# Kernel optimization log

Hardware: AMD Instinct MI355X
Metric: run time of the kernel (lower is better)

The kernel has to match this reference:

```python
import jax, jax.numpy as jnp
import numpy as np

N, C, IMG, HEADS = 512, 3, 32, 4
F = C * IMG * IMG          # 3072 node feature dim
E = 4096                   # edges without self loops
EPS = 1e-5                 # BatchNorm eps
SLOPE = 0.2                # GATv2 LeakyReLU negative slope


def bn(x, g, b, m, v):
    # eval-mode BatchNorm2d over channel dim 1
    inv = g / jnp.sqrt(v + EPS)
    return x * inv[None, :, None, None] + (b - m * inv)[None, :, None, None]


def conv1x1(x, W, b):
    # W: [out_c, in_c]
    return jnp.einsum('bchw,oc->bohw', x, W) + b[None, :, None, None]


def setup_inputs():
    key = jax.random.key(0)
    ks = jax.random.split(key, 32)
    inp = {}
    inp['x'] = jax.random.normal(ks[0], (N, C, IMG, IMG), jnp.float32)
    src = jax.random.randint(ks[1], (E,), 0, N)
    off = jax.random.randint(ks[2], (E,), 1, N)
    inp['edge_index'] = jnp.stack([src, (src + off) % N]).astype(jnp.int32)  # no self loops

    def w(k, shape, fan_in):
        return jax.random.normal(k, shape, jnp.float32) / np.sqrt(fan_in)

    i = 3
    def nk():
        nonlocal i; i += 1; return ks[i - 1]
    # grapher fc1: Conv2d(C,C,1)+BN
    inp['fc1_W'] = w(nk(), (C, C), C); inp['fc1_b'] = jnp.zeros((C,), jnp.float32)
    inp['bn1_g'] = jnp.ones((C,), jnp.float32); inp['bn1_b'] = jnp.zeros((C,), jnp.float32)
    inp['bn1_m'] = 0.1 * jax.random.normal(nk(), (C,), jnp.float32)
    inp['bn1_v'] = jax.random.uniform(nk(), (C,), jnp.float32, 0.5, 1.5)
    # GATv2Conv(F, F, heads=HEADS): lin_l, lin_r [F, HEADS*F] with bias, att [HEADS, F], out bias
    inp['Wl'] = w(nk(), (F, HEADS * F), F); inp['bl'] = jnp.zeros((HEADS * F,), jnp.float32)
    inp['Wr'] = w(nk(), (F, HEADS * F), F); inp['br'] = jnp.zeros((HEADS * F,), jnp.float32)
    inp['att'] = w(nk(), (HEADS, F), F)
    inp['gat_b'] = jnp.zeros((HEADS * F,), jnp.float32)
    # grapher fc2: Conv2d(C*HEADS, C, 1)+BN
    inp['fc2_W'] = w(nk(), (C, C * HEADS), C * HEADS); inp['fc2_b'] = jnp.zeros((C,), jnp.float32)
    inp['bn2_g'] = jnp.ones((C,), jnp.float32); inp['bn2_b'] = jnp.zeros((C,), jnp.float32)
    inp['bn2_m'] = 0.1 * jax.random.normal(nk(), (C,), jnp.float32)
    inp['bn2_v'] = jax.random.uniform(nk(), (C,), jnp.float32, 0.5, 1.5)
    # FFN fc1 / fc2 (C->C 1x1 conv + BN)
    inp['ffn1_W'] = w(nk(), (C, C), C); inp['ffn1_b'] = jnp.zeros((C,), jnp.float32)
    inp['bnf1_g'] = jnp.ones((C,), jnp.float32); inp['bnf1_b'] = jnp.zeros((C,), jnp.float32)
    inp['bnf1_m'] = 0.1 * jax.random.normal(nk(), (C,), jnp.float32)
    inp['bnf1_v'] = jax.random.uniform(nk(), (C,), jnp.float32, 0.5, 1.5)
    inp['ffn2_W'] = w(nk(), (C, C), C); inp['ffn2_b'] = jnp.zeros((C,), jnp.float32)
    inp['bnf2_g'] = jnp.ones((C,), jnp.float32); inp['bnf2_b'] = jnp.zeros((C,), jnp.float32)
    inp['bnf2_m'] = 0.1 * jax.random.normal(nk(), (C,), jnp.float32)
    inp['bnf2_v'] = jax.random.uniform(nk(), (C,), jnp.float32, 0.5, 1.5)
    return inp


def reference(x, edge_index, fc1_W, fc1_b, bn1_g, bn1_b, bn1_m, bn1_v,
              Wl, bl, Wr, br, att, gat_b,
              fc2_W, fc2_b, bn2_g, bn2_b, bn2_m, bn2_v,
              ffn1_W, ffn1_b, bnf1_g, bnf1_b, bnf1_m, bnf1_v,
              ffn2_W, ffn2_b, bnf2_g, bnf2_b, bnf2_m, bnf2_v):
    shortcut = x
    h = bn(conv1x1(x, fc1_W, fc1_b), bn1_g, bn1_b, bn1_m, bn1_v)
    hf = h.reshape(N, F)
    xl = (hf @ Wl + bl).reshape(N, HEADS, F)  # source transform
    xr = (hf @ Wr + br).reshape(N, HEADS, F)  # target transform
    # add self loops (PyG GATv2Conv default)
    loops = jnp.arange(N, dtype=edge_index.dtype)
    src = jnp.concatenate([edge_index[0], loops])
    dst = jnp.concatenate([edge_index[1], loops])
    # GATv2 edge scores: a . LeakyReLU(xl_j + xr_i)
    e = jax.nn.leaky_relu(xl[src] + xr[dst], negative_slope=SLOPE)  # [E+N, HEADS, F]
    logits = jnp.einsum('ehf,hf->eh', e, att)
    mx = jax.ops.segment_max(logits, dst, num_segments=N)
    ex = jnp.exp(logits - jax.lax.stop_gradient(mx)[dst])
    denom = jax.ops.segment_sum(ex, dst, num_segments=N)
    alpha = ex / denom[dst]                                          # segment softmax over targets
    agg = jax.ops.segment_sum(xl[src] * alpha[:, :, None], dst, num_segments=N)  # [N, HEADS, F]
    g_out = (agg.reshape(N, HEADS * F) + gat_b).reshape(N, C * HEADS, IMG, IMG)
    g = bn(conv1x1(g_out, fc2_W, fc2_b), bn2_g, bn2_b, bn2_m, bn2_v) + shortcut
    # FFN with residual
    f = jax.nn.relu(bn(conv1x1(g, ffn1_W, ffn1_b), bnf1_g, bnf1_b, bnf1_m, bnf1_v))
    f = bn(conv1x1(f, ffn2_W, ffn2_b), bnf2_g, bnf2_b, bnf2_m, bnf2_v)
    return f + g
```

## Files before the change

### kernel.cpp

```cpp
#include <hip/hip_runtime.h>

#define N_NODES 512
#define FDIM    3072
#define HEADS   4
#define HFD     12288
#define E_IN    4096
#define E_TOT   4608
#define EPSV    1e-5f
#define SLOPE   0.2f

typedef unsigned short u16;
typedef unsigned int   u32;

typedef short s16x8 __attribute__((ext_vector_type(8)));
typedef float f32x4 __attribute__((ext_vector_type(4)));

__device__ __forceinline__ u16 f2bf(float f){
  u32 u = __builtin_bit_cast(u32, f);
  u = (u + 0x7fffu + ((u >> 16) & 1u)) >> 16;
  return (u16)u;
}
__device__ __forceinline__ float bf2f(u16 h){
  return __builtin_bit_cast(float, ((u32)h) << 16);
}
__device__ __forceinline__ float bflo(u32 p){
  return __builtin_bit_cast(float, p << 16);
}
__device__ __forceinline__ float bfhi(u32 p){
  return __builtin_bit_cast(float, p & 0xffff0000u);
}

__device__ __forceinline__ void gl_lds16(const u16* g, u16* l){
  __builtin_amdgcn_global_load_lds(
      (const __attribute__((address_space(1))) unsigned int*)g,
      (__attribute__((address_space(3))) unsigned int*)l, 16, 0, 0);
}

__global__ void k_fc1(const float* __restrict__ x, const float* __restrict__ W,
                      const float* __restrict__ b, const float* __restrict__ g,
                      const float* __restrict__ bb, const float* __restrict__ m,
                      const float* __restrict__ v, u16* __restrict__ hf,
                      int* __restrict__ cnt){
  int id = blockIdx.x * 256 + threadIdx.x;
  if (id < 512) cnt[id] = 0;
  int n = id >> 10, p = id & 1023;
  float x0 = x[n * FDIM + p];
  float x1 = x[n * FDIM + 1024 + p];
  float x2 = x[n * FDIM + 2048 + p];
#pragma unroll
  for (int c = 0; c < 3; ++c){
    float t = b[c] + W[c*3+0]*x0 + W[c*3+1]*x1 + W[c*3+2]*x2;
    float inv = g[c] * rsqrtf(v[c] + EPSV);
    float o = t * inv + (bb[c] - m[c] * inv);
    hf[n * FDIM + c * 1024 + p] = f2bf(o);
  }
}

__global__ __launch_bounds__(256, 2) void k_gemm(
    const u16* __restrict__ hf, const float* __restrict__ Wl,
    const float* __restrict__ bl, const float* __restrict__ Wr,
    const float* __restrict__ br, u16* __restrict__ xl, u16* __restrict__ xr){
  __shared__ u16 As[512 * 32];
  __shared__ u16 Bs[64 * 40];

  const int tid  = threadIdx.x;
  const int wave = tid >> 6, lane = tid & 63;
  const int quad = lane >> 4, l16 = lane & 15;
  const int n0 = blockIdx.x * 64;

  const float* Wg; const float* biasp; u16* outp; int cb;
  if (n0 < HFD){ Wg = Wl; biasp = bl; outp = xl; cb = n0; }
  else         { Wg = Wr; biasp = br; outp = xr; cb = n0 - HFD; }

  const u16* ga = hf + (size_t)(wave * 128 + (lane >> 2)) * FDIM
                     + (((lane & 3) ^ ((lane >> 3) & 3)) << 3);
  u16* la = As + wave * 8 * 512;

  const int bn = tid & 63, bkh = tid >> 6;
  const float* gb = Wg + (size_t)bkh * 8 * HFD + (cb + bn);
  u16* wb = Bs + bn * 40 + bkh * 8;

  const u16* raf = As + (size_t)(wave * 128 + l16) * 32 + ((quad ^ ((l16 >> 1) & 3)) << 3);
  const u16* rbf = Bs + l16 * 40 + quad * 8;

  f32x4 acc[8][4];
#pragma unroll
  for (int i = 0; i < 8; ++i)
#pragma unroll
    for (int j = 0; j < 4; ++j) acc[i][j] = (f32x4){0.f, 0.f, 0.f, 0.f};

  float bv[8];
#pragma unroll
  for (int j = 0; j < 8; ++j) bv[j] = gb[(size_t)j * HFD];

  for (int ks = 0; ks < 96; ++ks){
    __syncthreads();
#pragma unroll
    for (int i = 0; i < 8; ++i)
      gl_lds16(ga + (size_t)i * 16 * FDIM + ks * 32, la + i * 512);
    u32 pk0 = (u32)f2bf(bv[0]) | ((u32)f2bf(bv[1]) << 16);
    u32 pk1 = (u32)f2bf(bv[2]) | ((u32)f2bf(bv[3]) << 16);
    u32 pk2 = (u32)f2bf(bv[4]) | ((u32)f2bf(bv[5]) << 16);
    u32 pk3 = (u32)f2bf(bv[6]) | ((u32)f2bf(bv[7]) << 16);
    *(uint4*)wb = make_uint4(pk0, pk1, pk2, pk3);
    __syncthreads();

    s16x8 af[8], bfr[4];
#pragma unroll
    for (int i = 0; i < 8; ++i)
      af[i] = __builtin_bit_cast(s16x8, *(const uint4*)(raf + i * 512));
#pragma unroll
    for (int j = 0; j < 4; ++j)
      bfr[j] = __builtin_bit_cast(s16x8, *(const uint4*)(rbf + j * 640));

    const int kn = (ks < 95 ? ks + 1 : ks) * 32;
#pragma unroll
    for (int j = 0; j < 8; ++j) bv[j] = gb[(size_t)(kn + j) * HFD];

#pragma unroll
    for (int i = 0; i < 8; ++i)
#pragma unroll
      for (int j = 0; j < 4; ++j)
        acc[i][j] = __builtin_amdgcn_mfma_f32_16x16x32_bf16(af[i], bfr[j], acc[i][j], 0, 0, 0);
  }

  float bj[4];
#pragma unroll
  for (int j = 0; j < 4; ++j) bj[j] = biasp[cb + j * 16 + l16];
#pragma unroll
  for (int i = 0; i < 8; ++i){
    int mrow = wave * 128 + i * 16 + quad * 4;
#pragma unroll
    for (int r = 0; r < 4; ++r){
      u16* orow = outp + (size_t)(mrow + r) * HFD + cb + l16;
#pragma unroll
      for (int j = 0; j < 4; ++j)
        orow[j * 16] = f2bf(acc[i][j][r] + bj[j]);
    }
  }
}

__global__ void k_logits(const int* __restrict__ ei, const u16* __restrict__ xl,
                         const u16* __restrict__ xr, const float* __restrict__ att,
                         float* __restrict__ logits, int* __restrict__ cnt){
  int e = blockIdx.x;
  int h = threadIdx.x >> 6, lane = threadIdx.x & 63;
  int s, d;
  if (e < E_IN){ s = ei[e]; d = ei[E_IN + e]; } else { s = e - E_IN; d = s; }
  if (threadIdx.x == 0) atomicAdd(&cnt[d], 1);
  const u16* xlp = xl + (size_t)s * HFD + h * FDIM;
  const u16* xrp = xr + (size_t)d * HFD + h * FDIM;
  const float* ap = att + h * FDIM;
  float acc = 0.f;
#pragma unroll
  for (int it = 0; it < 6; ++it){
    int f = it * 512 + lane * 8;
    uint4 a = *(const uint4*)(xlp + f);
    uint4 b = *(const uint4*)(xrp + f);
    float4 w0 = *(const float4*)(ap + f);
    float4 w1 = *(const float4*)(ap + f + 4);
    float v0 = bflo(a.x) + bflo(b.x); v0 = v0 > 0.f ? v0 : SLOPE * v0;
    float v1 = bfhi(a.x) + bfhi(b.x); v1 = v1 > 0.f ? v1 : SLOPE * v1;
    float v2 = bflo(a.y) + bflo(b.y); v2 = v2 > 0.f ? v2 : SLOPE * v2;
    float v3 = bfhi(a.y) + bfhi(b.y); v3 = v3 > 0.f ? v3 : SLOPE * v3;
    float v4 = bflo(a.z) + bflo(b.z); v4 = v4 > 0.f ? v4 : SLOPE * v4;
    float v5 = bfhi(a.z) + bfhi(b.z); v5 = v5 > 0.f ? v5 : SLOPE * v5;
    float v6 = bflo(a.w) + bflo(b.w); v6 = v6 > 0.f ? v6 : SLOPE * v6;
    float v7 = bfhi(a.w) + bfhi(b.w); v7 = v7 > 0.f ? v7 : SLOPE * v7;
    acc += v0 * w0.x + v1 * w0.y + v2 * w0.z + v3 * w0.w;
    acc += v4 * w1.x + v5 * w1.y + v6 * w1.z + v7 * w1.w;
  }
#pragma unroll
  for (int o = 32; o > 0; o >>= 1) acc += __shfl_down(acc, o);
  if (lane == 0) logits[e * 4 + h] = acc;
}

__global__ void k_scan(const int* __restrict__ cnt, int* __restrict__ off,
                       int* __restrict__ cursor){
  __shared__ int s[512];
  int t = threadIdx.x;
  int v = cnt[t];
  s[t] = v;
  __syncthreads();
  for (int d = 1; d < 512; d <<= 1){
    int add = (t >= d) ? s[t - d] : 0;
    __syncthreads();
    s[t] += add;
    __syncthreads();
  }
  int exc = s[t] - v;
  off[t] = exc;
  cursor[t] = exc;
}

__global__ void k_scatter(const int* __restrict__ ei, int* __restrict__ cursor,
                          int* __restrict__ elist){
  int e = blockIdx.x * 256 + threadIdx.x;
  if (e >= E_TOT) return;
  int d = (e < E_IN) ? ei[E_IN + e] : (e - E_IN);
  int pos = atomicAdd(&cursor[d], 1);
  elist[pos] = e;
}

__global__ void k_softmax(const int* __restrict__ cnt, const int* __restrict__ off,
                          const int* __restrict__ elist, const float* __restrict__ logits,
                          float* __restrict__ alpha){
  int i = blockIdx.x;
  int lane = threadIdx.x;
  int deg = cnt[i], st = off[i];
#pragma unroll
  for (int h = 0; h < 4; ++h){
    float mx = -1e30f;
    for (int j = lane; j < deg; j += 64){
      int e = elist[st + j];
      mx = fmaxf(mx, logits[e * 4 + h]);
    }
#pragma unroll
    for (int o = 32; o > 0; o >>= 1) mx = fmaxf(mx, __shfl_down(mx, o));
    mx = __shfl(mx, 0);
    float sm = 0.f;
    for (int j = lane; j < deg; j += 64){
      int e = elist[st + j];
      sm += __expf(logits[e * 4 + h] - mx);
    }
#pragma unroll
    for (int o = 32; o > 0; o >>= 1) sm += __shfl_down(sm, o);
    sm = __shfl(sm, 0);
    float rs = 1.f / sm;
    for (int j = lane; j < deg; j += 64){
      int e = elist[st + j];
      alpha[e * 4 + h] = __expf(logits[e * 4 + h] - mx) * rs;
    }
  }
}

__global__ void k_agg(const int* __restrict__ ei, const int* __restrict__ cnt,
                      const int* __restrict__ off, const int* __restrict__ elist,
                      const float* __restrict__ alpha, const u16* __restrict__ xl,
                      float* __restrict__ agg){
  int b = blockIdx.x;
  int dst = b >> 2, h = b & 3;
  int deg = cnt[dst], st = off[dst];
  int t = threadIdx.x;
#pragma unroll
  for (int c = 0; c < 3; ++c){
    int f = c * 1024 + t * 4;
    float a0 = 0.f, a1 = 0.f, a2 = 0.f, a3 = 0.f;
    for (int j = 0; j < deg; ++j){
      int e = elist[st + j];
      int s = (e < E_IN) ? ei[e] : (e - E_IN);
      float al = alpha[e * 4 + h];
      ushort4 xv = *(const ushort4*)(xl + (size_t)s * HFD + h * FDIM + f);
      a0 += al * bf2f(xv.x);
      a1 += al * bf2f(xv.y);
      a2 += al * bf2f(xv.z);
      a3 += al * bf2f(xv.w);
    }
    float4* op = (float4*)(agg + (size_t)dst * HFD + h * FDIM + f);
    *op = make_float4(a0, a1, a2, a3);
  }
}

__global__ void k_final(const float* __restrict__ agg, const float* __restrict__ gat_b,
                        const float* __restrict__ W2, const float* __restrict__ b2,
                        const float* __restrict__ g2, const float* __restrict__ bb2,
                        const float* __restrict__ m2, const float* __restrict__ v2,
                        const float* __restrict__ W3, const float* __restrict__ b3,
                        const float* __restrict__ g3, const float* __restrict__ bb3,
                        const float* __restrict__ m3, const float* __restrict__ v3,
                        const float* __restrict__ W4, const float* __restrict__ b4,
                        const float* __restrict__ g4, const float* __restrict__ bb4,
                        const float* __restrict__ m4, const float* __restrict__ v4,
                        const float* __restrict__ x, float* __restrict__ out){
  int id = blockIdx.x * 256 + threadIdx.x;
  int n = id >> 10, p = id & 1023;
  float a[12];
#pragma unroll
  for (int o = 0; o < 12; ++o)
    a[o] = agg[(size_t)n * HFD + o * 1024 + p] + gat_b[o * 1024 + p];
  float g[3];
#pragma unroll
  for (int c = 0; c < 3; ++c){
    float t = b2[c];
#pragma unroll
    for (int o = 0; o < 12; ++o) t += W2[c * 12 + o] * a[o];
    float inv = g2[c] * rsqrtf(v2[c] + EPSV);
    g[c] = t * inv + (bb2[c] - m2[c] * inv) + x[n * FDIM + c * 1024 + p];
  }
  float f1[3];
#pragma unroll
  for (int c = 0; c < 3; ++c){
    float t = b3[c] + W3[c*3+0]*g[0] + W3[c*3+1]*g[1] + W3[c*3+2]*g[2];
    float inv = g3[c] * rsqrtf(v3[c] + EPSV);
    float vv = t * inv + (bb3[c] - m3[c] * inv);
    f1[c] = fmaxf(vv, 0.f);
  }
#pragma unroll
  for (int c = 0; c < 3; ++c){
    float t = b4[c] + W4[c*3+0]*f1[0] + W4[c*3+1]*f1[1] + W4[c*3+2]*f1[2];
    float inv = g4[c] * rsqrtf(v4[c] + EPSV);
    out[n * FDIM + c * 1024 + p] = t * inv + (bb4[c] - m4[c] * inv) + g[c];
  }
}

extern "C" void kernel_launch(void* const* d_in, const int* in_sizes, int n_in,
                              void* d_out, int out_size, void* d_ws, size_t ws_size,
                              hipStream_t stream){
  (void)in_sizes; (void)n_in; (void)out_size; (void)ws_size;
  const float* x     = (const float*)d_in[0];
  const int*   ei    = (const int*)d_in[1];
  const float* fc1_W = (const float*)d_in[2];
  const float* fc1_b = (const float*)d_in[3];
  const float* bn1_g = (const float*)d_in[4];
  const float* bn1_b = (const float*)d_in[5];
  const float* bn1_m = (const float*)d_in[6];
  const float* bn1_v = (const float*)d_in[7];
  const float* Wl    = (const float*)d_in[8];
  const float* bl    = (const float*)d_in[9];
  const float* Wr    = (const float*)d_in[10];
  const float* br    = (const float*)d_in[11];
  const float* att   = (const float*)d_in[12];
  const float* gat_b = (const float*)d_in[13];
  const float* fc2_W = (const float*)d_in[14];
  const float* fc2_b = (const float*)d_in[15];
  const float* bn2_g = (const float*)d_in[16];
  const float* bn2_b = (const float*)d_in[17];
  const float* bn2_m = (const float*)d_in[18];
  const float* bn2_v = (const float*)d_in[19];
  const float* ffn1_W= (const float*)d_in[20];
  const float* ffn1_b= (const float*)d_in[21];
  const float* bnf1_g= (const float*)d_in[22];
  const float* bnf1_b= (const float*)d_in[23];
  const float* bnf1_m= (const float*)d_in[24];
  const float* bnf1_v= (const float*)d_in[25];
  const float* ffn2_W= (const float*)d_in[26];
  const float* ffn2_b= (const float*)d_in[27];
  const float* bnf2_g= (const float*)d_in[28];
  const float* bnf2_b= (const float*)d_in[29];
  const float* bnf2_m= (const float*)d_in[30];
  const float* bnf2_v= (const float*)d_in[31];

  char* w = (char*)d_ws;
  u16*   hf     = (u16*)(w);
  u16*   xl     = (u16*)(w + 3145728);
  u16*   xr     = (u16*)(w + 15728640);
  float* logits = (float*)(w + 28311552);
  float* alpha  = (float*)(w + 28385280);
  int*   cnt    = (int*)(w + 28459008);
  int*   offp   = (int*)(w + 28461056);
  int*   cursor = (int*)(w + 28463104);
  int*   elist  = (int*)(w + 28465152);
  float* agg    = (float*)(w + 28483584);

  k_fc1<<<2048, 256, 0, stream>>>(x, fc1_W, fc1_b, bn1_g, bn1_b, bn1_m, bn1_v, hf, cnt);
  k_gemm<<<384, 256, 0, stream>>>(hf, Wl, bl, Wr, br, xl, xr);
  k_logits<<<E_TOT, 256, 0, stream>>>(ei, xl, xr, att, logits, cnt);
  k_scan<<<1, 512, 0, stream>>>(cnt, offp, cursor);
  k_scatter<<<18, 256, 0, stream>>>(ei, cursor, elist);
  k_softmax<<<512, 64, 0, stream>>>(cnt, offp, elist, logits, alpha);
  k_agg<<<2048, 256, 0, stream>>>(ei, cnt, offp, elist, alpha, xl, agg);
  k_final<<<2048, 256, 0, stream>>>(agg, gat_b, fc2_W, fc2_b, bn2_g, bn2_b, bn2_m, bn2_v,
                                    ffn1_W, ffn1_b, bnf1_g, bnf1_b, bnf1_m, bnf1_v,
                                    ffn2_W, ffn2_b, bnf2_g, bnf2_b, bnf2_m, bnf2_v,
                                    x, (float*)d_out);
}
```

Measured before the change: 553.4 us.

## Double-buffer GEMM with M-split tiles, fuse scan/scatter and agg/final kernels

The projection GEMM now splits M into two halves per block (768 blocks, smaller accumulators, launch bounds 3). It double-buffers LDS so the next k-slice loads overlap the MFMA work, and uses one barrier per step plus a grouped tile order. The scan and scatter kernels merge into one kernel that uses an LDS cursor. Aggregation and the fc2/FFN epilogue merge into a per-node kernel, which removes the float agg buffer round trip. The risks are fewer blocks and more registers in the fused aggregation (48 accumulators per thread), and serial atomics in the single-block scatter.

```diff
diff --git a/kernel.cpp b/kernel.cpp
--- a/kernel.cpp
+++ b/kernel.cpp
@@ -56,80 +56,104 @@
   }
 }
 
-__global__ __launch_bounds__(256, 2) void k_gemm(
+__global__ __launch_bounds__(256, 3) void k_gemm(
     const u16* __restrict__ hf, const float* __restrict__ Wl,
     const float* __restrict__ bl, const float* __restrict__ Wr,
     const float* __restrict__ br, u16* __restrict__ xl, u16* __restrict__ xr){
-  __shared__ u16 As[512 * 32];
-  __shared__ u16 Bs[64 * 40];
+  __shared__ u16 As[2][256 * 32];
+  __shared__ u16 Bs[2][64 * 40];
 
   const int tid  = threadIdx.x;
   const int wave = tid >> 6, lane = tid & 63;
   const int quad = lane >> 4, l16 = lane & 15;
-  const int n0 = blockIdx.x * 64;
+
+  const int g = blockIdx.x;
+  const int ntile = (g >> 4) * 8 + (g & 7);
+  const int mhalf = (g >> 3) & 1;
+  const int n0 = ntile * 64;
+  const int rbase = mhalf * 256;
 
   const float* Wg; const float* biasp; u16* outp; int cb;
   if (n0 < HFD){ Wg = Wl; biasp = bl; outp = xl; cb = n0; }
   else         { Wg = Wr; biasp = br; outp = xr; cb = n0 - HFD; }
 
-  const u16* ga = hf + (size_t)(wave * 128 + (lane >> 2)) * FDIM
+  const u16* ga = hf + (size_t)(rbase + wave * 64 + (lane >> 2)) * FDIM
                      + (((lane & 3) ^ ((lane >> 3) & 3)) << 3);
-  u16* la = As + wave * 8 * 512;
 
   const int bn = tid & 63, bkh = tid >> 6;
   const float* gb = Wg + (size_t)bkh * 8 * HFD + (cb + bn);
-  u16* wb = Bs + bn * 40 + bkh * 8;
-
-  const u16* raf = As + (size_t)(wave * 128 + l16) * 32 + ((quad ^ ((l16 >> 1) & 3)) << 3);
-  const u16* rbf = Bs + l16 * 40 + quad * 8;
-
-  f32x4 acc[8][4];
-#pragma unroll
-  for (int i = 0; i < 8; ++i)
+  const int bwo = bn * 40 + bkh * 8;
+
+  const int araw = (wave * 64 + l16) * 32 + ((quad ^ ((l16 >> 1) & 3)) << 3);
+  const int brd  = l16 * 40 + quad * 8;
+
+  f32x4 acc[4][4];
+#pragma unroll
+  for (int i = 0; i < 4; ++i)
 #pragma unroll
     for (int j = 0; j < 4; ++j) acc[i][j] = (f32x4){0.f, 0.f, 0.f, 0.f};
 
   float bv[8];
 #pragma unroll
   for (int j = 0; j < 8; ++j) bv[j] = gb[(size_t)j * HFD];
-
-  for (int ks = 0; ks < 96; ++ks){
-    __syncthreads();
-#pragma unroll
-    for (int i = 0; i < 8; ++i)
-      gl_lds16(ga + (size_t)i * 16 * FDIM + ks * 32, la + i * 512);
-    u32 pk0 = (u32)f2bf(bv[0]) | ((u32)f2bf(bv[1]) << 16);
-    u32 pk1 = (u32)f2bf(bv[2]) | ((u32)f2bf(bv[3]) << 16);
-    u32 pk2 = (u32)f2bf(bv[4]) | ((u32)f2bf(bv[5]) << 16);
-    u32 pk3 = (u32)f2bf(bv[6]) | ((u32)f2bf(bv[7]) << 16);
-    *(uint4*)wb = make_uint4(pk0, pk1, pk2, pk3);
-    __syncthreads();
-
-    s16x8 af[8], bfr[4];
-#pragma unroll
-    for (int i = 0; i < 8; ++i)
-      af[i] = __builtin_bit_cast(s16x8, *(const uint4*)(raf + i * 512));
-#pragma unroll
-    for (int j = 0; j < 4; ++j)
-      bfr[j] = __builtin_bit_cast(s16x8, *(const uint4*)(rbf + j * 640));
-
-    const int kn = (ks < 95 ? ks + 1 : ks) * 32;
-#pragma unroll
-    for (int j = 0; j < 8; ++j) bv[j] = gb[(size_t)(kn + j) * HFD];
-
-#pragma unroll
-    for (int i = 0; i < 8; ++i)
-#pragma unroll
-      for (int j = 0; j < 4; ++j)
-        acc[i][j] = __builtin_amdgcn_mfma_f32_16x16x32_bf16(af[i], bfr[j], acc[i][j], 0, 0, 0);
-  }
+#pragma unroll
+  for (int i = 0; i < 4; ++i)
+    gl_lds16(ga + (size_t)i * 16 * FDIM, As[0] + (wave * 4 + i) * 512);
+  {
+    u32 p0 = (u32)f2bf(bv[0]) | ((u32)f2bf(bv[1]) << 16);
+    u32 p1 = (u32)f2bf(bv[2]) | ((u32)f2bf(bv[3]) << 16);
+    u32 p2 = (u32)f2bf(bv[4]) | ((u32)f2bf(bv[5]) << 16);
+    u32 p3 = (u32)f2bf(bv[6]) | ((u32)f2bf(bv[7]) << 16);
+    *(uint4*)(Bs[0] + bwo) = make_uint4(p0, p1, p2, p3);
+  }
+#pragma unroll
+  for (int j = 0; j < 8; ++j) bv[j] = gb[(size_t)(32 + j) * HFD];
+  __syncthreads();
+
+#define GEMM_BODY(KS, CUR, NXT)                                               \
+  {                                                                           \
+    const int ksv = (KS);                                                     \
+    if (ksv < 95){                                                            \
+      _Pragma("unroll")                                                       \
+      for (int i = 0; i < 4; ++i)                                             \
+        gl_lds16(ga + (size_t)i * 16 * FDIM + (ksv + 1) * 32,                 \
+                 As[NXT] + (wave * 4 + i) * 512);                             \
+      u32 p0 = (u32)f2bf(bv[0]) | ((u32)f2bf(bv[1]) << 16);                   \
+      u32 p1 = (u32)f2bf(bv[2]) | ((u32)f2bf(bv[3]) << 16);                   \
+      u32 p2 = (u32)f2bf(bv[4]) | ((u32)f2bf(bv[5]) << 16);                   \
+      u32 p3 = (u32)f2bf(bv[6]) | ((u32)f2bf(bv[7]) << 16);                   \
+      *(uint4*)(Bs[NXT] + bwo) = make_uint4(p0, p1, p2, p3);                  \
+      int kn = (ksv + 2 < 96 ? ksv + 2 : 95) * 32;                            \
+      _Pragma("unroll")                                                       \
+      for (int j = 0; j < 8; ++j) bv[j] = gb[(size_t)(kn + j) * HFD];         \
+    }                                                                         \
+    s16x8 af[4], bfr[4];                                                      \
+    _Pragma("unroll")                                                         \
+    for (int i = 0; i < 4; ++i)                                               \
+      af[i] = __builtin_bit_cast(s16x8, *(const uint4*)(As[CUR] + araw + i * 512)); \
+    _Pragma("unroll")                                                         \
+    for (int j = 0; j < 4; ++j)                                               \
+      bfr[j] = __builtin_bit_cast(s16x8, *(const uint4*)(Bs[CUR] + brd + j * 640)); \
+    _Pragma("unroll")                                                         \
+    for (int i = 0; i < 4; ++i)                                               \
+      _Pragma("unroll")                                                       \
+      for (int j = 0; j < 4; ++j)                                             \
+        acc[i][j] = __builtin_amdgcn_mfma_f32_16x16x32_bf16(af[i], bfr[j], acc[i][j], 0, 0, 0); \
+    __syncthreads();                                                          \
+  }
+
+  for (int ks = 0; ks < 96; ks += 2){
+    GEMM_BODY(ks, 0, 1);
+    GEMM_BODY(ks + 1, 1, 0);
+  }
+#undef GEMM_BODY
 
   float bj[4];
 #pragma unroll
   for (int j = 0; j < 4; ++j) bj[j] = biasp[cb + j * 16 + l16];
 #pragma unroll
-  for (int i = 0; i < 8; ++i){
-    int mrow = wave * 128 + i * 16 + quad * 4;
+  for (int i = 0; i < 4; ++i){
+    int mrow = rbase + wave * 64 + i * 16 + quad * 4;
 #pragma unroll
     for (int r = 0; r < 4; ++r){
       u16* orow = outp + (size_t)(mrow + r) * HFD + cb + l16;
@@ -175,9 +199,10 @@
   if (lane == 0) logits[e * 4 + h] = acc;
 }
 
-__global__ void k_scan(const int* __restrict__ cnt, int* __restrict__ off,
-                       int* __restrict__ cursor){
+__global__ void k_scan_scatter(const int* __restrict__ ei, const int* __restrict__ cnt,
+                               int* __restrict__ off, int* __restrict__ elist){
   __shared__ int s[512];
+  __shared__ int cur[512];
   int t = threadIdx.x;
   int v = cnt[t];
   s[t] = v;
@@ -190,16 +215,13 @@
   }
   int exc = s[t] - v;
   off[t] = exc;
-  cursor[t] = exc;
-}
-
-__global__ void k_scatter(const int* __restrict__ ei, int* __restrict__ cursor,
-                          int* __restrict__ elist){
-  int e = blockIdx.x * 256 + threadIdx.x;
-  if (e >= E_TOT) return;
-  int d = (e < E_IN) ? ei[E_IN + e] : (e - E_IN);
-  int pos = atomicAdd(&cursor[d], 1);
-  elist[pos] = e;
+  cur[t] = exc;
+  __syncthreads();
+  for (int e = t; e < E_TOT; e += 512){
+    int d = (e < E_IN) ? ei[E_IN + e] : (e - E_IN);
+    int pos = atomicAdd(&cur[d], 1);
+    elist[pos] = e;
+  }
 }
 
 __global__ void k_softmax(const int* __restrict__ cnt, const int* __restrict__ off,
@@ -234,73 +256,104 @@
   }
 }
 
-__global__ void k_agg(const int* __restrict__ ei, const int* __restrict__ cnt,
-                      const int* __restrict__ off, const int* __restrict__ elist,
-                      const float* __restrict__ alpha, const u16* __restrict__ xl,
-                      float* __restrict__ agg){
-  int b = blockIdx.x;
-  int dst = b >> 2, h = b & 3;
-  int deg = cnt[dst], st = off[dst];
-  int t = threadIdx.x;
+__global__ __launch_bounds__(256) void k_aggfinal(
+    const int* __restrict__ ei, const int* __restrict__ cnt,
+    const int* __restrict__ off, const int* __restrict__ elist,
+    const float* __restrict__ alpha, const u16* __restrict__ xl,
+    const float* __restrict__ gat_b,
+    const float* __restrict__ W2, const float* __restrict__ b2,
+    const float* __restrict__ g2, const float* __restrict__ bb2,
+    const float* __restrict__ m2, const float* __restrict__ v2,
+    const float* __restrict__ W3, const float* __restrict__ b3,
+    const float* __restrict__ g3, const float* __restrict__ bb3,
+    const float* __restrict__ m3, const float* __restrict__ v3,
+    const float* __restrict__ W4, const float* __restrict__ b4,
+    const float* __restrict__ g4, const float* __restrict__ bb4,
+    const float* __restrict__ m4, const float* __restrict__ v4,
+    const float* __restrict__ x, float* __restrict__ out){
+  __shared__ int    s_src[128];
+  __shared__ float4 s_al[128];
+  const int n = blockIdx.x;
+  const int t = threadIdx.x;
+  const int p4 = t * 4;
+  const int deg = cnt[n], st = off[n];
+
+  float acc[12][4];
+#pragma unroll
+  for (int o = 0; o < 12; ++o)
+#pragma unroll
+    for (int r = 0; r < 4; ++r) acc[o][r] = 0.f;
+
+  for (int base = 0; base < deg; base += 128){
+    int cn = min(deg - base, 128);
+    if (t < cn){
+      int e = elist[st + base + t];
+      s_src[t] = (e < E_IN) ? ei[e] : (e - E_IN);
+      s_al[t] = *(const float4*)(alpha + e * 4);
+    }
+    __syncthreads();
+    for (int j = 0; j < cn; ++j){
+      int s = s_src[j];
+      float4 al4 = s_al[j];
+      float alh[4] = {al4.x, al4.y, al4.z, al4.w};
+      const u16* bp = xl + (size_t)s * HFD;
+#pragma unroll
+      for (int h = 0; h < 4; ++h){
+#pragma unroll
+        for (int c = 0; c < 3; ++c){
+          ushort4 xv = *(const ushort4*)(bp + h * FDIM + c * 1024 + p4);
+          acc[h*3+c][0] += alh[h] * bf2f(xv.x);
+          acc[h*3+c][1] += alh[h] * bf2f(xv.y);
+          acc[h*3+c][2] += alh[h] * bf2f(xv.z);
+          acc[h*3+c][3] += alh[h] * bf2f(xv.w);
+        }
+      }
+    }
+    __syncthreads();
+  }
+
+#pragma unroll
+  for (int o = 0; o < 12; ++o){
+    float4 gv = *(const float4*)(gat_b + o * 1024 + p4);
+    acc[o][0] += gv.x; acc[o][1] += gv.y; acc[o][2] += gv.z; acc[o][3] += gv.w;
+  }
+  float xv[3][4];
 #pragma unroll
   for (int c = 0; c < 3; ++c){
-    int f = c * 1024 + t * 4;
-    float a0 = 0.f, a1 = 0.f, a2 = 0.f, a3 = 0.f;
-    for (int j = 0; j < deg; ++j){
-      int e = elist[st + j];
-      int s = (e < E_IN) ? ei[e] : (e - E_IN);
-      float al = alpha[e * 4 + h];
-      ushort4 xv = *(const ushort4*)(xl + (size_t)s * HFD + h * FDIM + f);
-      a0 += al * bf2f(xv.x);
-      a1 += al * bf2f(xv.y);
-      a2 += al * bf2f(xv.z);
-      a3 += al * bf2f(xv.w);
-    }
-    float4* op = (float4*)(agg + (size_t)dst * HFD + h * FDIM + f);
-    *op = make_float4(a0, a1, a2, a3);
-  }
-}
-
-__global__ void k_final(const float* __restrict__ agg, const float* __restrict__ gat_b,
-                        const float* __restrict__ W2, const float* __restrict__ b2,
-                        const float* __restrict__ g2, const float* __restrict__ bb2,
-                        const float* __restrict__ m2, const float* __restrict__ v2,
-                        const float* __restrict__ W3, const float* __restrict__ b3,
-                        const float* __restrict__ g3, const float* __restrict__ bb3,
-                        const float* __restrict__ m3, const float* __restrict__ v3,
-                        const float* __restrict__ W4, const float* __restrict__ b4,
-                        const float* __restrict__ g4, const float* __restrict__ bb4,
-                        const float* __restrict__ m4, const float* __restrict__ v4,
-                        const float* __restrict__ x, float* __restrict__ out){
-  int id = blockIdx.x * 256 + threadIdx.x;
-  int n = id >> 10, p = id & 1023;
-  float a[12];
-#pragma unroll
-  for (int o = 0; o < 12; ++o)
-    a[o] = agg[(size_t)n * HFD + o * 1024 + p] + gat_b[o * 1024 + p];
-  float g[3];
-#pragma unroll
-  for (int c = 0; c < 3; ++c){
-    float t = b2[c];
-#pragma unroll
-    for (int o = 0; o < 12; ++o) t += W2[c * 12 + o] * a[o];
-    float inv = g2[c] * rsqrtf(v2[c] + EPSV);
-    g[c] = t * inv + (bb2[c] - m2[c] * inv) + x[n * FDIM + c * 1024 + p];
-  }
-  float f1[3];
-#pragma unroll
-  for (int c = 0; c < 3; ++c){
-    float t = b3[c] + W3[c*3+0]*g[0] + W3[c*3+1]*g[1] + W3[c*3+2]*g[2];
-    float inv = g3[c] * rsqrtf(v3[c] + EPSV);
-    float vv = t * inv + (bb3[c] - m3[c] * inv);
-    f1[c] = fmaxf(vv, 0.f);
-  }
-#pragma unroll
-  for (int c = 0; c < 3; ++c){
-    float t = b4[c] + W4[c*3+0]*f1[0] + W4[c*3+1]*f1[1] + W4[c*3+2]*f1[2];
-    float inv = g4[c] * rsqrtf(v4[c] + EPSV);
-    out[n * FDIM + c * 1024 + p] = t * inv + (bb4[c] - m4[c] * inv) + g[c];
-  }
+    float4 t4 = *(const float4*)(x + (size_t)n * FDIM + c * 1024 + p4);
+    xv[c][0] = t4.x; xv[c][1] = t4.y; xv[c][2] = t4.z; xv[c][3] = t4.w;
+  }
+  float o4[3][4];
+#pragma unroll
+  for (int r = 0; r < 4; ++r){
+    float gch[3];
+#pragma unroll
+    for (int c = 0; c < 3; ++c){
+      float tt = b2[c];
+#pragma unroll
+      for (int o = 0; o < 12; ++o) tt += W2[c * 12 + o] * acc[o][r];
+      float inv = g2[c] * rsqrtf(v2[c] + EPSV);
+      gch[c] = tt * inv + (bb2[c] - m2[c] * inv) + xv[c][r];
+    }
+    float f1[3];
+#pragma unroll
+    for (int c = 0; c < 3; ++c){
+      float tt = b3[c] + W3[c*3+0]*gch[0] + W3[c*3+1]*gch[1] + W3[c*3+2]*gch[2];
+      float inv = g3[c] * rsqrtf(v3[c] + EPSV);
+      float vv = tt * inv + (bb3[c] - m3[c] * inv);
+      f1[c] = fmaxf(vv, 0.f);
+    }
+#pragma unroll
+    for (int c = 0; c < 3; ++c){
+      float tt = b4[c] + W4[c*3+0]*f1[0] + W4[c*3+1]*f1[1] + W4[c*3+2]*f1[2];
+      float inv = g4[c] * rsqrtf(v4[c] + EPSV);
+      o4[c][r] = tt * inv + (bb4[c] - m4[c] * inv) + gch[c];
+    }
+  }
+#pragma unroll
+  for (int c = 0; c < 3; ++c)
+    *(float4*)(out + (size_t)n * FDIM + c * 1024 + p4) =
+        make_float4(o4[c][0], o4[c][1], o4[c][2], o4[c][3]);
 }
 
 extern "C" void kernel_launch(void* const* d_in, const int* in_sizes, int n_in,
@@ -348,19 +401,16 @@
   float* alpha  = (float*)(w + 28385280);
   int*   cnt    = (int*)(w + 28459008);
   int*   offp   = (int*)(w + 28461056);
-  int*   cursor = (int*)(w + 28463104);
   int*   elist  = (int*)(w + 28465152);
-  float* agg    = (float*)(w + 28483584);
 
   k_fc1<<<2048, 256, 0, stream>>>(x, fc1_W, fc1_b, bn1_g, bn1_b, bn1_m, bn1_v, hf, cnt);
-  k_gemm<<<384, 256, 0, stream>>>(hf, Wl, bl, Wr, br, xl, xr);
+  k_gemm<<<768, 256, 0, stream>>>(hf, Wl, bl, Wr, br, xl, xr);
   k_logits<<<E_TOT, 256, 0, stream>>>(ei, xl, xr, att, logits, cnt);
-  k_scan<<<1, 512, 0, stream>>>(cnt, offp, cursor);
-  k_scatter<<<18, 256, 0, stream>>>(ei, cursor, elist);
+  k_scan_scatter<<<1, 512, 0, stream>>>(ei, cnt, offp, elist);
   k_softmax<<<512, 64, 0, stream>>>(cnt, offp, elist, logits, alpha);
-  k_agg<<<2048, 256, 0, stream>>>(ei, cnt, offp, elist, alpha, xl, agg);
-  k_final<<<2048, 256, 0, stream>>>(agg, gat_b, fc2_W, fc2_b, bn2_g, bn2_b, bn2_m, bn2_v,
-                                    ffn1_W, ffn1_b, bnf1_g, bnf1_b, bnf1_m, bnf1_v,
-                                    ffn2_W, ffn2_b, bnf2_g, bnf2_b, bnf2_m, bnf2_v,
-                                    x, (float*)d_out);
-}
+  k_aggfinal<<<512, 256, 0, stream>>>(ei, cnt, offp, elist, alpha, xl, gat_b,
+                                      fc2_W, fc2_b, bn2_g, bn2_b, bn2_m, bn2_v,
+                                      ffn1_W, ffn1_b, bnf1_g, bnf1_b, bnf1_m, bnf1_v,
+                                      ffn2_W, ffn2_b, bnf2_g, bnf2_b, bnf2_m, bnf2_v,
+                                      x, (float*)d_out);
+}
```

Measured after the change: 527.1 us. 1.05x faster.
